# Kernel optimization log

Hardware: AMD Instinct MI355X
Metric: run time of the kernel (lower is better)

Reference implementation:

```python
import jax, jax.numpy as jnp
import numpy as np

S, M, E, K, D = 16384, 512, 16, 2, 256
H1, H2, H3 = 500, 500, 1000


def setup_inputs() -> dict:
    key = jax.random.key(0)
    ks = jax.random.split(key, 8)
    p = lambda k, sh: jax.random.normal(k, sh, dtype=jnp.float32) * 0.02
    return {
        "x": jax.random.normal(ks[0], (S, M), dtype=jnp.float32),
        "noise": jax.random.uniform(ks[1], (S, E), dtype=jnp.float32),  # Router's torch.rand noise
        "Wr": p(ks[2], (E, M)),                       # router weight (Linear, no bias)
        "W1": p(ks[3], (E, M, H1)), "b1": jnp.zeros((E, H1), jnp.float32),
        "W2": p(ks[4], (E, H1, H2)), "b2": jnp.zeros((E, H2), jnp.float32),
        "W3": p(ks[5], (E, H2, H3)), "b3": jnp.zeros((E, H3), jnp.float32),
        "W4": p(ks[6], (E, H3, D)), "b4": jnp.zeros((E, D), jnp.float32),
    }


def reference(x, noise, Wr, W1, b1, W2, b2, W3, b3, W4, b4):
    # Router: zero-init linear + uniform noise
    logits = x @ Wr.T + noise                      # [S,E]
    select = jax.nn.softmax(logits, axis=1)        # [S,E]
    gate, index = jax.lax.top_k(select, K)         # [S,K]
    gate = gate / gate.sum(axis=1, keepdims=True)
    mask = jax.nn.one_hot(index, E, dtype=jnp.float32)  # [S,K,E]

    # load-balance loss
    density = mask.sum(axis=1).mean(axis=0)        # [E]
    density_proxy = select.mean(axis=0)            # [E]
    balance_loss = (density_proxy * density).mean() * float(E ** 2)

    # combine tensor: mask_flat is all-ones, so combine = sum_k gate_k * one_hot_k
    final_weight = (gate[:, :, None] * mask).sum(axis=1)     # [S,E]
    dispatch = (final_weight > 0).astype(x.dtype)            # bool->float, [S,E]
    select0 = dispatch

    # dense one-hot dispatch: expert_inputs[e,s,:] = x[s,:] * dispatch[s,e]
    expert_inputs = jnp.einsum('sm,se->esm', x, dispatch)    # [E,S,M]

    # per-expert Encoder MLP, vectorized over experts
    h = jax.nn.relu(jnp.einsum('esm,emh->esh', expert_inputs, W1) + b1[:, None, :])
    h = jax.nn.relu(jnp.einsum('esh,ehg->esg', h, W2) + b2[:, None, :])
    h = jax.nn.relu(jnp.einsum('esg,egf->esf', h, W3) + b3[:, None, :])
    expert_out = jnp.einsum('esf,efd->esd', h, W4) + b4[:, None, :]  # [E,S,D]

    final_output = jnp.einsum('se,esd->sd', final_weight, expert_out)  # [S,D]
    dist_loss = jnp.float32(0.0)  # t=False path
    return final_output, select0, balance_loss, dist_loss
```

## Files before the change

### kernel.cpp

```cpp
#include <hip/hip_runtime.h>
#include <stdint.h>

#define S_TOK 16384
#define M_DIM 512
#define E_EXP 16
#define D_OUT 256
#define H1D 500
#define H2D 500
#define H3D 1000

typedef float f32x4 __attribute__((ext_vector_type(4)));
typedef long lx2 __attribute__((ext_vector_type(2)));
typedef int i32x2 __attribute__((ext_vector_type(2)));

template <bool HI>
__device__ __forceinline__ int pk8(float a, float b, int old) {
  return __builtin_amdgcn_cvt_pk_fp8_f32(a, b, old, HI);
}
__device__ __forceinline__ unsigned char f2fp8(float f) {
  return (unsigned char)(__builtin_amdgcn_cvt_pk_fp8_f32(f, 0.f, 0, false) & 0xff);
}

__device__ __forceinline__ void ld_lds16(const unsigned char* g, unsigned char* l) {
  __builtin_amdgcn_global_load_lds(
      (const __attribute__((address_space(1))) unsigned int*)(const void*)g,
      (__attribute__((address_space(3))) unsigned int*)(void*)l, 16, 0, 0);
}

struct TokenRec { int i1, i2; float g1, g2; };

__global__ __launch_bounds__(256) void k_router(const float* __restrict__ x,
                                                const float* __restrict__ noise,
                                                const float* __restrict__ Wr,
                                                float* __restrict__ sel_out,
                                                float* __restrict__ sel_buf,
                                                TokenRec* __restrict__ te) {
  __shared__ float wr[E_EXP * 516];
  int t = threadIdx.x;
  for (int i = t; i < E_EXP * M_DIM; i += 256) {
    int e = i >> 9, m = i & 511;
    wr[e * 516 + m] = Wr[i];
  }
  __syncthreads();

  int wv = t >> 6, l = t & 63;
  int e = l & 15, tg = l >> 4;
  int s = blockIdx.x * 16 + wv * 4 + tg;

  const float* xr = x + (size_t)s * M_DIM;
  const float* wre = &wr[e * 516];
  double a0 = 0.0, a1 = 0.0, a2 = 0.0, a3 = 0.0;
#pragma unroll 4
  for (int m = 0; m < M_DIM; m += 4) {
    f32x4 xv = *(const f32x4*)(xr + m);
    f32x4 wv4 = *(const f32x4*)(wre + m);
    a0 += (double)xv.x * (double)wv4.x;
    a1 += (double)xv.y * (double)wv4.y;
    a2 += (double)xv.z * (double)wv4.z;
    a3 += (double)xv.w * (double)wv4.w;
  }
  double a = (a0 + a1) + (a2 + a3);
  a += (double)noise[(size_t)s * E_EXP + e];

  double mx = a;
#pragma unroll
  for (int off = 8; off >= 1; off >>= 1) { double o = __shfl_xor(mx, off, 64); mx = (o > mx) ? o : mx; }
  double p = exp(a - mx);
  double sum = p;
#pragma unroll
  for (int off = 8; off >= 1; off >>= 1) sum += __shfl_xor(sum, off, 64);
  sel_buf[(size_t)s * E_EXP + e] = (float)(p / sum);

  unsigned long long pb = __double_as_longlong(p);
  unsigned long long key = (pb & ~0xFFull) | (unsigned long long)(255 - e);
  unsigned long long k1 = key;
#pragma unroll
  for (int off = 8; off >= 1; off >>= 1) { unsigned long long o = __shfl_xor(k1, off, 64); k1 = (o > k1) ? o : k1; }
  int i1 = 255 - (int)(k1 & 0xFFull);
  unsigned long long key2 = (e == i1) ? 0ull : key;
  unsigned long long k2 = key2;
#pragma unroll
  for (int off = 8; off >= 1; off >>= 1) { unsigned long long o = __shfl_xor(k2, off, 64); k2 = (o > k2) ? o : k2; }
  int i2 = 255 - (int)(k2 & 0xFFull);

  double p1 = __shfl(p, tg * 16 + i1, 64);
  double p2 = __shfl(p, tg * 16 + i2, 64);

  sel_out[(size_t)s * E_EXP + e] = (e == i1 || e == i2) ? 1.f : 0.f;
  if (e == 0) {
    double inv = 1.0 / (p1 + p2);
    TokenRec r; r.i1 = i1; r.i2 = i2; r.g1 = (float)(p1 * inv); r.g2 = (float)(p2 * inv);
    te[s] = r;
  }
}

__global__ __launch_bounds__(256) void k_stats(const float* __restrict__ sel_buf,
                                               const TokenRec* __restrict__ te,
                                               float* __restrict__ partials) {
  __shared__ float psum[256];
  __shared__ unsigned int hist[E_EXP];
  int t = threadIdx.x, b = blockIdx.x;
  if (t < E_EXP) hist[t] = 0u;
  __syncthreads();
  int e = t & 15, rg = t >> 4;
  int base = b * 1024;
  float acc = 0.f;
#pragma unroll 4
  for (int i = 0; i < 64; i++)
    acc += sel_buf[(size_t)(base + i * 16 + rg) * E_EXP + e];
  for (int i = t; i < 1024; i += 256) {
    TokenRec r = te[base + i];
    atomicAdd(&hist[r.i1], 1u);
    atomicAdd(&hist[r.i2], 1u);
  }
  psum[t] = acc;
  __syncthreads();
  if (t < E_EXP) {
    float v = 0.f;
#pragma unroll
    for (int rg2 = 0; rg2 < 16; rg2++) v += psum[rg2 * 16 + t];
    partials[b * 32 + t] = v;
    partials[b * 32 + 16 + t] = (float)hist[t];
  }
}

__global__ void k_prefix_loss(const float* __restrict__ partials,
                              unsigned int* __restrict__ counts,
                              unsigned int* __restrict__ offsets,
                              unsigned int* __restrict__ cursor,
                              float* __restrict__ out_loss) {
  __shared__ float pr[E_EXP];
  __shared__ unsigned int cn[E_EXP];
  int t = threadIdx.x;
  if (t < E_EXP) {
    float p = 0.f, c = 0.f;
    for (int b = 0; b < 16; b++) { p += partials[b * 32 + t]; c += partials[b * 32 + 16 + t]; }
    pr[t] = p; cn[t] = (unsigned int)(c + 0.5f);
    cursor[t] = 0u;
  }
  __syncthreads();
  if (t == 0) {
    unsigned int acc = 0; float ls = 0.f;
    for (int e = 0; e < E_EXP; e++) {
      counts[e] = cn[e];
      offsets[e] = acc;
      acc += cn[e];
      ls += pr[e] * (float)cn[e];
    }
    out_loss[0] = ls * ((float)E_EXP / ((float)S_TOK * (float)S_TOK));
    out_loss[1] = 0.f;
  }
}

__global__ __launch_bounds__(256) void k_listbuild(const TokenRec* __restrict__ te,
                                                   const unsigned int* __restrict__ offsets,
                                                   unsigned int* __restrict__ cursor,
                                                   int* __restrict__ slot_token,
                                                   float* __restrict__ slot_gate,
                                                   int* __restrict__ tok_slot) {
  __shared__ unsigned int lhist[E_EXP];
  __shared__ unsigned int lbase[E_EXP];
  __shared__ unsigned int lcur[E_EXP];
  int t = threadIdx.x, b = blockIdx.x;
  int base = b * 1024;
  if (t < E_EXP) lhist[t] = 0u;
  __syncthreads();
  for (int i = t; i < 1024; i += 256) {
    TokenRec r = te[base + i];
    atomicAdd(&lhist[r.i1], 1u);
    atomicAdd(&lhist[r.i2], 1u);
  }
  __syncthreads();
  if (t < E_EXP) {
    lbase[t] = offsets[t] + atomicAdd(&cursor[t], lhist[t]);
    lcur[t] = 0u;
  }
  __syncthreads();
  for (int i = t; i < 1024; i += 256) {
    int s = base + i;
    TokenRec r = te[s];
    unsigned int p1 = atomicAdd(&lcur[r.i1], 1u);
    int sl1 = (int)(lbase[r.i1] + p1);
    slot_token[sl1] = s; slot_gate[sl1] = r.g1;
    unsigned int p2 = atomicAdd(&lcur[r.i2], 1u);
    int sl2 = (int)(lbase[r.i2] + p2);
    slot_token[sl2] = s; slot_gate[sl2] = r.g2;
    tok_slot[2 * s] = sl1;
    tok_slot[2 * s + 1] = sl2;
  }
}

__global__ __launch_bounds__(256) void k_gather(const float* __restrict__ x,
                                                const int* __restrict__ slot_token,
                                                unsigned char* __restrict__ xg) {
  int idx = blockIdx.x * 256 + threadIdx.x;
  int row = idx >> 6, t6 = idx & 63;
  int blk = t6 >> 3, q = (t6 >> 1) & 3, h = t6 & 1;
  int tkn = slot_token[row];
  const float* xp = x + (size_t)tkn * M_DIM + blk * 64 + h * 32 + q * 8;
  f32x4 v0 = *(const f32x4*)xp;
  f32x4 v1 = *(const f32x4*)(xp + 4);
  int b0 = pk8<false>(v0.x, v0.y, 0); b0 = pk8<true>(v0.z, v0.w, b0);
  int b1 = pk8<false>(v1.x, v1.y, 0); b1 = pk8<true>(v1.z, v1.w, b1);
  i32x2 o; o.x = b0; o.y = b1;
  *(i32x2*)&xg[(size_t)row * 512 + blk * 64 + q * 16 + h * 8] = o;
}

__global__ __launch_bounds__(256) void k_convw_all(const float* __restrict__ W1,
                                                   const float* __restrict__ W2,
                                                   const float* __restrict__ W3,
                                                   const float* __restrict__ W4,
                                                   unsigned char* __restrict__ D1,
                                                   unsigned char* __restrict__ D2,
                                                   unsigned char* __restrict__ D3,
                                                   unsigned char* __restrict__ D4) {
  __shared__ float tile[64][65];
  int tb = blockIdx.x, e = blockIdx.y;
  const float* src; unsigned char* dst;
  int Kr, Nr, Kp, Np, kx, ny;
  if (tb < 64)        { src = W1; dst = D1; Kr = 512;  Nr = H1D; Kp = 512;  Np = 512;  kx = tb >> 3;  ny = tb & 7; }
  else if (tb < 128)  { tb -= 64;  src = W2; dst = D2; Kr = H1D; Nr = H2D; Kp = 512;  Np = 512;  kx = tb >> 3;  ny = tb & 7; }
  else if (tb < 256)  { tb -= 128; src = W3; dst = D3; Kr = H2D; Nr = H3D; Kp = 512;  Np = 1024; kx = tb >> 4;  ny = tb & 15; }
  else                { tb -= 256; src = W4; dst = D4; Kr = H3D; Nr = 256; Kp = 1024; Np = 256;  kx = tb >> 2;  ny = tb & 3; }
  int k0 = kx * 64, n0 = ny * 64;
  int t = threadIdx.x;
  int cx = t & 63, ry = t >> 6;
  const float* sp = src + (size_t)e * Kr * Nr;
#pragma unroll
  for (int i = 0; i < 16; i++) {
    int k = k0 + ry + i * 4, n = n0 + cx;
    float v = (k < Kr && n < Nr) ? sp[(size_t)k * Nr + n] : 0.f;
    tile[ry + i * 4][cx] = v;
  }
  __syncthreads();
  int nl = t >> 2, q = t & 3;
  int b0 = pk8<false>(tile[q * 8 + 0][nl], tile[q * 8 + 1][nl], 0);
  b0 = pk8<true>(tile[q * 8 + 2][nl], tile[q * 8 + 3][nl], b0);
  int b1 = pk8<false>(tile[q * 8 + 4][nl], tile[q * 8 + 5][nl], 0);
  b1 = pk8<true>(tile[q * 8 + 6][nl], tile[q * 8 + 7][nl], b1);
  int c0 = pk8<false>(tile[32 + q * 8 + 0][nl], tile[32 + q * 8 + 1][nl], 0);
  c0 = pk8<true>(tile[32 + q * 8 + 2][nl], tile[32 + q * 8 + 3][nl], c0);
  int c1 = pk8<false>(tile[32 + q * 8 + 4][nl], tile[32 + q * 8 + 5][nl], 0);
  c1 = pk8<true>(tile[32 + q * 8 + 6][nl], tile[32 + q * 8 + 7][nl], c1);
  uint4 pk; pk.x = (unsigned)b0; pk.y = (unsigned)b1; pk.z = (unsigned)c0; pk.w = (unsigned)c1;
  *(uint4*)&dst[(size_t)e * Np * Kp + (size_t)(n0 + nl) * Kp + k0 + q * 16] = pk;
}

__global__ __launch_bounds__(256, 4) void k_gemm_mid(const unsigned char* __restrict__ in,
                                                  const unsigned char* __restrict__ wt,
                                                  const float* __restrict__ bias,
                                                  unsigned char* __restrict__ out,
                                                  const unsigned int* __restrict__ offsets,
                                                  const unsigned int* __restrict__ counts,
                                                  int KP, int NP, int NREAL) {
  int e = blockIdx.z;
  int n_e = (int)counts[e];
  if (n_e == 0) return;
  int base = (int)offsets[e];
  int bn = blockIdx.y;
  __shared__ __align__(16) unsigned char As[2][128 * 64];
  __shared__ __align__(16) unsigned char Bs[2][64 * 64];
  int t = threadIdx.x;
  int w = t >> 6, l = t & 63;
  int wm = w & 1, wn = w >> 1;
  int lr = l & 15, lq = l >> 4;
  int r_ = l >> 2, s_ = l & 3;
  int s2 = s_ ^ ((r_ >> 1) & 3);
  int rsw = (lq ^ ((lr >> 1) & 3)) * 16;
  int c0 = w * 2, c1 = w * 2 + 1;

  unsigned char* dA0[2] = {&As[0][c0 * 1024], &As[1][c0 * 1024]};
  unsigned char* dA1[2] = {&As[0][c1 * 1024], &As[1][c1 * 1024]};
  unsigned char* dB[2]  = {&Bs[0][w * 1024], &Bs[1][w * 1024]};

  const unsigned char* bW = wt + (size_t)e * NP * KP;
  const unsigned char* bsrc = bW + (size_t)(bn * 64 + w * 16 + r_) * KP + s2 * 16;
  int nk = KP >> 6;

  for (int bm = blockIdx.x; bm * 128 < n_e; bm += gridDim.x) {
    int ra = bm * 128 + c0 * 16 + r_; ra = (ra < n_e) ? ra : (n_e - 1);
    int rb = bm * 128 + c1 * 16 + r_; rb = (rb < n_e) ? rb : (n_e - 1);
    const unsigned char* a0 = in + (size_t)(base + ra) * KP + s2 * 16;
    const unsigned char* a1 = in + (size_t)(base + rb) * KP + s2 * 16;
    const unsigned char* bq = bsrc;
    f32x4 acc[4][2];
#pragma unroll
    for (int i = 0; i < 4; i++)
#pragma unroll
      for (int j = 0; j < 2; j++) acc[i][j] = (f32x4){0.f, 0.f, 0.f, 0.f};

    ld_lds16(a0, dA0[0]); ld_lds16(a1, dA1[0]); ld_lds16(bq, dB[0]);
    a0 += 64; a1 += 64; bq += 64;

    for (int ks = 0; ks < nk; ks++) {
      int cb = ks & 1, nb = cb ^ 1;
      __syncthreads();
      if (ks + 1 < nk) {
        ld_lds16(a0, dA0[nb]); ld_lds16(a1, dA1[nb]); ld_lds16(bq, dB[nb]);
        a0 += 64; a1 += 64; bq += 64;
      }
      lx2 af[4], bf[2];
#pragma unroll
      for (int mt = 0; mt < 4; mt++) af[mt] = *(const lx2*)&As[cb][(wm * 64 + mt * 16 + lr) * 64 + rsw];
#pragma unroll
      for (int nt = 0; nt < 2; nt++) bf[nt] = *(const lx2*)&Bs[cb][(wn * 32 + nt * 16 + lr) * 64 + rsw];
#pragma unroll
      for (int mt = 0; mt < 4; mt++)
#pragma unroll
        for (int nt = 0; nt < 2; nt++) {
          acc[mt][nt] = __builtin_amdgcn_mfma_f32_16x16x32_fp8_fp8(af[mt].x, bf[nt].x, acc[mt][nt], 0, 0, 0);
          acc[mt][nt] = __builtin_amdgcn_mfma_f32_16x16x32_fp8_fp8(af[mt].y, bf[nt].y, acc[mt][nt], 0, 0, 0);
        }
    }

#pragma unroll
    for (int nt = 0; nt < 2; nt++) {
      int col = bn * 64 + wn * 32 + nt * 16 + lr;
      bool cok = col < NREAL;
      float bv = cok ? bias[(size_t)e * NREAL + col] : 0.f;
      int kl = col & 63;
      int pb = ((kl >> 3) & 3) * 16 + ((kl >> 5) & 1) * 8 + (kl & 7);
#pragma unroll
      for (int mt = 0; mt < 4; mt++)
#pragma unroll
        for (int reg = 0; reg < 4; reg++) {
          int r = bm * 128 + wm * 64 + mt * 16 + lq * 4 + reg;
          if (r < n_e) {
            float v = cok ? fmaxf(acc[mt][nt][reg] + bv, 0.f) : 0.f;
            out[(size_t)(base + r) * NP + bn * 64 + pb] = f2fp8(v);
          }
        }
    }
  }
}

__global__ __launch_bounds__(256, 4) void k_gemm_fin(const unsigned char* __restrict__ in,
                                                  const unsigned char* __restrict__ wt,
                                                  const float* __restrict__ bias,
                                                  float* __restrict__ eo,
                                                  const unsigned int* __restrict__ offsets,
                                                  const unsigned int* __restrict__ counts,
                                                  const float* __restrict__ slot_gate) {
  const int KP = 1024, NP = 256;
  int e = blockIdx.z;
  int n_e = (int)counts[e];
  if (n_e == 0) return;
  int base = (int)offsets[e];
  int bn = blockIdx.y;
  __shared__ __align__(16) unsigned char As[2][64 * 64];
  __shared__ __align__(16) unsigned char Bs[2][64 * 64];
  int t = threadIdx.x;
  int w = t >> 6, l = t & 63;
  int wm = w & 1, wn = w >> 1;
  int lr = l & 15, lq = l >> 4;
  int r_ = l >> 2, s_ = l & 3;
  int s2 = s_ ^ ((r_ >> 1) & 3);
  int rsw = (lq ^ ((lr >> 1) & 3)) * 16;

  unsigned char* dA[2] = {&As[0][w * 1024], &As[1][w * 1024]};
  unsigned char* dB[2] = {&Bs[0][w * 1024], &Bs[1][w * 1024]};

  const unsigned char* bW = wt + (size_t)e * NP * KP;
  const unsigned char* bsrc = bW + (size_t)(bn * 64 + w * 16 + r_) * KP + s2 * 16;
  int nk = KP >> 6;

  for (int bm = blockIdx.x; bm * 64 < n_e; bm += gridDim.x) {
    int ra = bm * 64 + w * 16 + r_; ra = (ra < n_e) ? ra : (n_e - 1);
    const unsigned char* a0 = in + (size_t)(base + ra) * KP + s2 * 16;
    const unsigned char* bq = bsrc;
    f32x4 acc[2][2];
#pragma unroll
    for (int i = 0; i < 2; i++)
#pragma unroll
      for (int j = 0; j < 2; j++) acc[i][j] = (f32x4){0.f, 0.f, 0.f, 0.f};

    ld_lds16(a0, dA[0]); ld_lds16(bq, dB[0]);
    a0 += 64; bq += 64;

    for (int ks = 0; ks < nk; ks++) {
      int cb = ks & 1, nb = cb ^ 1;
      __syncthreads();
      if (ks + 1 < nk) {
        ld_lds16(a0, dA[nb]); ld_lds16(bq, dB[nb]);
        a0 += 64; bq += 64;
      }
      lx2 af[2], bf[2];
#pragma unroll
      for (int mt = 0; mt < 2; mt++) af[mt] = *(const lx2*)&As[cb][(wm * 32 + mt * 16 + lr) * 64 + rsw];
#pragma unroll
      for (int nt = 0; nt < 2; nt++) bf[nt] = *(const lx2*)&Bs[cb][(wn * 32 + nt * 16 + lr) * 64 + rsw];
#pragma unroll
      for (int mt = 0; mt < 2; mt++)
#pragma unroll
        for (int nt = 0; nt < 2; nt++) {
          acc[mt][nt] = __builtin_amdgcn_mfma_f32_16x16x32_fp8_fp8(af[mt].x, bf[nt].x, acc[mt][nt], 0, 0, 0);
          acc[mt][nt] = __builtin_amdgcn_mfma_f32_16x16x32_fp8_fp8(af[mt].y, bf[nt].y, acc[mt][nt], 0, 0, 0);
        }
    }

#pragma unroll
    for (int mt = 0; mt < 2; mt++)
#pragma unroll
      for (int reg = 0; reg < 4; reg++) {
        int r = bm * 64 + wm * 32 + mt * 16 + lq * 4 + reg;
        if (r < n_e) {
          int gr = base + r;
          float g = slot_gate[gr];
#pragma unroll
          for (int nt = 0; nt < 2; nt++) {
            int col = bn * 64 + wn * 32 + nt * 16 + lr;
            eo[(size_t)gr * NP + col] = g * (acc[mt][nt][reg] + bias[(size_t)e * 256 + col]);
          }
        }
      }
  }
}

__global__ __launch_bounds__(256) void k_combine(const float* __restrict__ eo,
                                                 const int* __restrict__ tok_slot,
                                                 float* __restrict__ out) {
  int idx = blockIdx.x * 256 + threadIdx.x;
  int s = idx >> 6, q = idx & 63;
  int sl1 = tok_slot[2 * s], sl2 = tok_slot[2 * s + 1];
  f32x4 v1 = *(const f32x4*)&eo[(size_t)sl1 * D_OUT + q * 4];
  f32x4 v2 = *(const f32x4*)&eo[(size_t)sl2 * D_OUT + q * 4];
  *(f32x4*)&out[(size_t)s * D_OUT + q * 4] = v1 + v2;
}

extern "C" void kernel_launch(void* const* d_in, const int* in_sizes, int n_in,
                              void* d_out, int out_size, void* d_ws, size_t ws_size,
                              hipStream_t stream) {
  const float* x    = (const float*)d_in[0];
  const float* nois = (const float*)d_in[1];
  const float* Wr   = (const float*)d_in[2];
  const float* W1   = (const float*)d_in[3];
  const float* b1   = (const float*)d_in[4];
  const float* W2   = (const float*)d_in[5];
  const float* b2   = (const float*)d_in[6];
  const float* W3   = (const float*)d_in[7];
  const float* b3   = (const float*)d_in[8];
  const float* W4   = (const float*)d_in[9];
  const float* b4   = (const float*)d_in[10];
  float* out = (float*)d_out;

  char* w = (char*)d_ws;
  unsigned char* actA = (unsigned char*)(w + 0);
  unsigned char* actB = (unsigned char*)(w + 33554432);
  unsigned char* Wt1  = (unsigned char*)(w + 50331648);
  unsigned char* Wt2  = (unsigned char*)(w + 54525952);
  unsigned char* Wt3  = (unsigned char*)(w + 58720256);
  unsigned char* Wt4  = (unsigned char*)(w + 67108864);
  float*         eo   = (float*)(w + 71303168);
  int*           slot_token = (int*)(w + 104857600);
  float*         slot_gate  = (float*)(w + 104988672);
  TokenRec*      te         = (TokenRec*)(w + 105119744);
  unsigned int*  counts  = (unsigned int*)(w + 105381888);
  unsigned int*  cursor  = (unsigned int*)(w + 105381952);
  unsigned int*  offsets = (unsigned int*)(w + 105382016);
  int*           tok_slot = (int*)(w + 105382080);
  float*         sel_buf  = (float*)(w + 0);
  float*         partials = (float*)(w + 1048576);

  float* sel_out  = out + (size_t)S_TOK * D_OUT;
  float* loss_out = out + (size_t)S_TOK * D_OUT + (size_t)S_TOK * E_EXP;

  k_convw_all<<<dim3(320, E_EXP), dim3(256), 0, stream>>>(W1, W2, W3, W4, Wt1, Wt2, Wt3, Wt4);

  k_router<<<dim3(S_TOK / 16), dim3(256), 0, stream>>>(x, nois, Wr, sel_out, sel_buf, te);
  k_stats<<<dim3(16), dim3(256), 0, stream>>>(sel_buf, te, partials);
  k_prefix_loss<<<dim3(1), dim3(64), 0, stream>>>(partials, counts, offsets, cursor, loss_out);
  k_listbuild<<<dim3(16), dim3(256), 0, stream>>>(te, offsets, cursor, slot_token, slot_gate, tok_slot);
  k_gather<<<dim3((2 * S_TOK * 64) / 256), dim3(256), 0, stream>>>(x, slot_token, actB);

  k_gemm_mid<<<dim3(24, 8, E_EXP), dim3(256), 0, stream>>>(actB, Wt1, b1, actA, offsets, counts, 512, 512, H1D);
  k_gemm_mid<<<dim3(24, 8, E_EXP), dim3(256), 0, stream>>>(actA, Wt2, b2, actB, offsets, counts, 512, 512, H2D);
  k_gemm_mid<<<dim3(24, 16, E_EXP), dim3(256), 0, stream>>>(actB, Wt3, b3, actA, offsets, counts, 512, 1024, H3D);
  k_gemm_fin<<<dim3(32, 4, E_EXP), dim3(256), 0, stream>>>(actA, Wt4, b4, eo, offsets, counts, slot_gate);
  k_combine<<<dim3(S_TOK * 64 / 256), dim3(256), 0, stream>>>(eo, tok_slot, out);

  (void)in_sizes; (void)n_in; (void)out_size; (void)ws_size;
}
```

Measured before the change: 382.3 us.

## Enlarge expert GEMM tiles to 128x128 and swap MFMA operands for packed epilogue stores

The middle expert GEMMs now use 128x128 output tiles, where each wave computes a 64x64 sub-tile, and the final GEMM uses 128x64 tiles instead of 64x64. The MFMA operand order is swapped so each lane holds four consecutive output columns. That lets the epilogue write packed 4-byte fp8 words and float4 outputs with vectorised bias loads, replacing scattered single-byte and single-float stores. The goal is more data reuse per LDS load and fewer store instructions. The cost is more accumulator registers, lower occupancy (launch bounds drop to 3) and fewer blocks in the grids.

```diff
diff --git a/kernel.cpp b/kernel.cpp
--- a/kernel.cpp
+++ b/kernel.cpp
@@ -246,13 +246,112 @@
   *(uint4*)&dst[(size_t)e * Np * Kp + (size_t)(n0 + nl) * Kp + k0 + q * 16] = pk;
 }
 
-__global__ __launch_bounds__(256, 4) void k_gemm_mid(const unsigned char* __restrict__ in,
+__global__ __launch_bounds__(256, 3) void k_gemm_mid(const unsigned char* __restrict__ in,
                                                   const unsigned char* __restrict__ wt,
                                                   const float* __restrict__ bias,
                                                   unsigned char* __restrict__ out,
                                                   const unsigned int* __restrict__ offsets,
                                                   const unsigned int* __restrict__ counts,
                                                   int KP, int NP, int NREAL) {
+  int e = blockIdx.z;
+  int n_e = (int)counts[e];
+  if (n_e == 0) return;
+  int base = (int)offsets[e];
+  int bn = blockIdx.y;
+  __shared__ __align__(16) unsigned char As[2][128 * 64];
+  __shared__ __align__(16) unsigned char Bs[2][128 * 64];
+  int t = threadIdx.x;
+  int w = t >> 6, l = t & 63;
+  int wm = w & 1, wn = w >> 1;
+  int lr = l & 15, lq = l >> 4;
+  int r_ = l >> 2, s_ = l & 3;
+  int s2 = s_ ^ ((r_ >> 1) & 3);
+  int rsw = (lq ^ ((lr >> 1) & 3)) * 16;
+  int c0 = 2 * w, c1 = 2 * w + 1;
+
+  unsigned char* dA0[2] = {&As[0][c0 * 1024], &As[1][c0 * 1024]};
+  unsigned char* dA1[2] = {&As[0][c1 * 1024], &As[1][c1 * 1024]};
+  unsigned char* dB0[2] = {&Bs[0][c0 * 1024], &Bs[1][c0 * 1024]};
+  unsigned char* dB1[2] = {&Bs[0][c1 * 1024], &Bs[1][c1 * 1024]};
+
+  const unsigned char* bW = wt + (size_t)e * NP * KP;
+  const unsigned char* bs0 = bW + (size_t)(bn * 128 + c0 * 16 + r_) * KP + s2 * 16;
+  const unsigned char* bs1 = bW + (size_t)(bn * 128 + c1 * 16 + r_) * KP + s2 * 16;
+  int nk = KP >> 6;
+
+  for (int bm = blockIdx.x; bm * 128 < n_e; bm += gridDim.x) {
+    int ra = bm * 128 + c0 * 16 + r_; ra = (ra < n_e) ? ra : (n_e - 1);
+    int rb = bm * 128 + c1 * 16 + r_; rb = (rb < n_e) ? rb : (n_e - 1);
+    const unsigned char* a0 = in + (size_t)(base + ra) * KP + s2 * 16;
+    const unsigned char* a1 = in + (size_t)(base + rb) * KP + s2 * 16;
+    const unsigned char* b0 = bs0;
+    const unsigned char* b1 = bs1;
+    f32x4 acc[4][4];
+#pragma unroll
+    for (int i = 0; i < 4; i++)
+#pragma unroll
+      for (int j = 0; j < 4; j++) acc[i][j] = (f32x4){0.f, 0.f, 0.f, 0.f};
+
+    ld_lds16(a0, dA0[0]); ld_lds16(a1, dA1[0]); ld_lds16(b0, dB0[0]); ld_lds16(b1, dB1[0]);
+    a0 += 64; a1 += 64; b0 += 64; b1 += 64;
+
+    for (int ks = 0; ks < nk; ks++) {
+      int cb = ks & 1, nb = cb ^ 1;
+      __syncthreads();
+      if (ks + 1 < nk) {
+        ld_lds16(a0, dA0[nb]); ld_lds16(a1, dA1[nb]); ld_lds16(b0, dB0[nb]); ld_lds16(b1, dB1[nb]);
+        a0 += 64; a1 += 64; b0 += 64; b1 += 64;
+      }
+      lx2 af[4], wf[4];
+#pragma unroll
+      for (int mi = 0; mi < 4; mi++) af[mi] = *(const lx2*)&As[cb][(wm * 64 + mi * 16 + lr) * 64 + rsw];
+#pragma unroll
+      for (int ni = 0; ni < 4; ni++) wf[ni] = *(const lx2*)&Bs[cb][(wn * 64 + ni * 16 + lr) * 64 + rsw];
+#pragma unroll
+      for (int ni = 0; ni < 4; ni++)
+#pragma unroll
+        for (int mi = 0; mi < 4; mi++) {
+          acc[ni][mi] = __builtin_amdgcn_mfma_f32_16x16x32_fp8_fp8(wf[ni].x, af[mi].x, acc[ni][mi], 0, 0, 0);
+          acc[ni][mi] = __builtin_amdgcn_mfma_f32_16x16x32_fp8_fp8(wf[ni].y, af[mi].y, acc[ni][mi], 0, 0, 0);
+        }
+    }
+
+    int mbase = bm * 128 + wm * 64;
+    int nbase = bn * 128 + wn * 64;
+#pragma unroll
+    for (int ni = 0; ni < 4; ni++) {
+      int n0 = nbase + ni * 16 + lq * 4;
+      bool cok = n0 < NREAL;
+      f32x4 bv = (f32x4){0.f, 0.f, 0.f, 0.f};
+      if (cok) bv = *(const f32x4*)&bias[(size_t)e * NREAL + n0];
+      int k6 = n0 & 63;
+      int off = (n0 >> 6) * 64 + ((k6 >> 3) & 3) * 16 + (k6 >> 5) * 8 + (k6 & 7);
+#pragma unroll
+      for (int mi = 0; mi < 4; mi++) {
+        int m = mbase + mi * 16 + lr;
+        if (m < n_e) {
+          unsigned int pkv = 0u;
+          if (cok) {
+            f32x4 v = acc[ni][mi];
+            int p = pk8<false>(fmaxf(v.x + bv.x, 0.f), fmaxf(v.y + bv.y, 0.f), 0);
+            p = pk8<true>(fmaxf(v.z + bv.z, 0.f), fmaxf(v.w + bv.w, 0.f), p);
+            pkv = (unsigned int)p;
+          }
+          *(unsigned int*)&out[(size_t)(base + m) * NP + off] = pkv;
+        }
+      }
+    }
+  }
+}
+
+__global__ __launch_bounds__(256, 4) void k_gemm_fin(const unsigned char* __restrict__ in,
+                                                  const unsigned char* __restrict__ wt,
+                                                  const float* __restrict__ bias,
+                                                  float* __restrict__ eo,
+                                                  const unsigned int* __restrict__ offsets,
+                                                  const unsigned int* __restrict__ counts,
+                                                  const float* __restrict__ slot_gate) {
+  const int KP = 1024, NP = 256;
   int e = blockIdx.z;
   int n_e = (int)counts[e];
   if (n_e == 0) return;
@@ -267,7 +366,7 @@
   int r_ = l >> 2, s_ = l & 3;
   int s2 = s_ ^ ((r_ >> 1) & 3);
   int rsw = (lq ^ ((lr >> 1) & 3)) * 16;
-  int c0 = w * 2, c1 = w * 2 + 1;
+  int c0 = 2 * w, c1 = 2 * w + 1;
 
   unsigned char* dA0[2] = {&As[0][c0 * 1024], &As[1][c0 * 1024]};
   unsigned char* dA1[2] = {&As[0][c1 * 1024], &As[1][c1 * 1024]};
@@ -283,11 +382,11 @@
     const unsigned char* a0 = in + (size_t)(base + ra) * KP + s2 * 16;
     const unsigned char* a1 = in + (size_t)(base + rb) * KP + s2 * 16;
     const unsigned char* bq = bsrc;
-    f32x4 acc[4][2];
-#pragma unroll
-    for (int i = 0; i < 4; i++)
-#pragma unroll
-      for (int j = 0; j < 2; j++) acc[i][j] = (f32x4){0.f, 0.f, 0.f, 0.f};
+    f32x4 acc[2][4];
+#pragma unroll
+    for (int i = 0; i < 2; i++)
+#pragma unroll
+      for (int j = 0; j < 4; j++) acc[i][j] = (f32x4){0.f, 0.f, 0.f, 0.f};
 
     ld_lds16(a0, dA0[0]); ld_lds16(a1, dA1[0]); ld_lds16(bq, dB[0]);
     a0 += 64; a1 += 64; bq += 64;
@@ -299,120 +398,41 @@
         ld_lds16(a0, dA0[nb]); ld_lds16(a1, dA1[nb]); ld_lds16(bq, dB[nb]);
         a0 += 64; a1 += 64; bq += 64;
       }
-      lx2 af[4], bf[2];
-#pragma unroll
-      for (int mt = 0; mt < 4; mt++) af[mt] = *(const lx2*)&As[cb][(wm * 64 + mt * 16 + lr) * 64 + rsw];
-#pragma unroll
-      for (int nt = 0; nt < 2; nt++) bf[nt] = *(const lx2*)&Bs[cb][(wn * 32 + nt * 16 + lr) * 64 + rsw];
-#pragma unroll
-      for (int mt = 0; mt < 4; mt++)
-#pragma unroll
-        for (int nt = 0; nt < 2; nt++) {
-          acc[mt][nt] = __builtin_amdgcn_mfma_f32_16x16x32_fp8_fp8(af[mt].x, bf[nt].x, acc[mt][nt], 0, 0, 0);
-          acc[mt][nt] = __builtin_amdgcn_mfma_f32_16x16x32_fp8_fp8(af[mt].y, bf[nt].y, acc[mt][nt], 0, 0, 0);
+      lx2 af[4], wf[2];
+#pragma unroll
+      for (int mi = 0; mi < 4; mi++) af[mi] = *(const lx2*)&As[cb][(wm * 64 + mi * 16 + lr) * 64 + rsw];
+#pragma unroll
+      for (int ni = 0; ni < 2; ni++) wf[ni] = *(const lx2*)&Bs[cb][(wn * 32 + ni * 16 + lr) * 64 + rsw];
+#pragma unroll
+      for (int ni = 0; ni < 2; ni++)
+#pragma unroll
+        for (int mi = 0; mi < 4; mi++) {
+          acc[ni][mi] = __builtin_amdgcn_mfma_f32_16x16x32_fp8_fp8(wf[ni].x, af[mi].x, acc[ni][mi], 0, 0, 0);
+          acc[ni][mi] = __builtin_amdgcn_mfma_f32_16x16x32_fp8_fp8(wf[ni].y, af[mi].y, acc[ni][mi], 0, 0, 0);
         }
     }
 
-#pragma unroll
-    for (int nt = 0; nt < 2; nt++) {
-      int col = bn * 64 + wn * 32 + nt * 16 + lr;
-      bool cok = col < NREAL;
-      float bv = cok ? bias[(size_t)e * NREAL + col] : 0.f;
-      int kl = col & 63;
-      int pb = ((kl >> 3) & 3) * 16 + ((kl >> 5) & 1) * 8 + (kl & 7);
-#pragma unroll
-      for (int mt = 0; mt < 4; mt++)
-#pragma unroll
-        for (int reg = 0; reg < 4; reg++) {
-          int r = bm * 128 + wm * 64 + mt * 16 + lq * 4 + reg;
-          if (r < n_e) {
-            float v = cok ? fmaxf(acc[mt][nt][reg] + bv, 0.f) : 0.f;
-            out[(size_t)(base + r) * NP + bn * 64 + pb] = f2fp8(v);
-          }
-        }
-    }
-  }
-}
-
-__global__ __launch_bounds__(256, 4) void k_gemm_fin(const unsigned char* __restrict__ in,
-                                                  const unsigned char* __restrict__ wt,
-                                                  const float* __restrict__ bias,
-                                                  float* __restrict__ eo,
-                                                  const unsigned int* __restrict__ offsets,
-                                                  const unsigned int* __restrict__ counts,
-                                                  const float* __restrict__ slot_gate) {
-  const int KP = 1024, NP = 256;
-  int e = blockIdx.z;
-  int n_e = (int)counts[e];
-  if (n_e == 0) return;
-  int base = (int)offsets[e];
-  int bn = blockIdx.y;
-  __shared__ __align__(16) unsigned char As[2][64 * 64];
-  __shared__ __align__(16) unsigned char Bs[2][64 * 64];
-  int t = threadIdx.x;
-  int w = t >> 6, l = t & 63;
-  int wm = w & 1, wn = w >> 1;
-  int lr = l & 15, lq = l >> 4;
-  int r_ = l >> 2, s_ = l & 3;
-  int s2 = s_ ^ ((r_ >> 1) & 3);
-  int rsw = (lq ^ ((lr >> 1) & 3)) * 16;
-
-  unsigned char* dA[2] = {&As[0][w * 1024], &As[1][w * 1024]};
-  unsigned char* dB[2] = {&Bs[0][w * 1024], &Bs[1][w * 1024]};
-
-  const unsigned char* bW = wt + (size_t)e * NP * KP;
-  const unsigned char* bsrc = bW + (size_t)(bn * 64 + w * 16 + r_) * KP + s2 * 16;
-  int nk = KP >> 6;
-
-  for (int bm = blockIdx.x; bm * 64 < n_e; bm += gridDim.x) {
-    int ra = bm * 64 + w * 16 + r_; ra = (ra < n_e) ? ra : (n_e - 1);
-    const unsigned char* a0 = in + (size_t)(base + ra) * KP + s2 * 16;
-    const unsigned char* bq = bsrc;
-    f32x4 acc[2][2];
-#pragma unroll
-    for (int i = 0; i < 2; i++)
-#pragma unroll
-      for (int j = 0; j < 2; j++) acc[i][j] = (f32x4){0.f, 0.f, 0.f, 0.f};
-
-    ld_lds16(a0, dA[0]); ld_lds16(bq, dB[0]);
-    a0 += 64; bq += 64;
-
-    for (int ks = 0; ks < nk; ks++) {
-      int cb = ks & 1, nb = cb ^ 1;
-      __syncthreads();
-      if (ks + 1 < nk) {
-        ld_lds16(a0, dA[nb]); ld_lds16(bq, dB[nb]);
-        a0 += 64; bq += 64;
-      }
-      lx2 af[2], bf[2];
-#pragma unroll
-      for (int mt = 0; mt < 2; mt++) af[mt] = *(const lx2*)&As[cb][(wm * 32 + mt * 16 + lr) * 64 + rsw];
-#pragma unroll
-      for (int nt = 0; nt < 2; nt++) bf[nt] = *(const lx2*)&Bs[cb][(wn * 32 + nt * 16 + lr) * 64 + rsw];
-#pragma unroll
-      for (int mt = 0; mt < 2; mt++)
-#pragma unroll
-        for (int nt = 0; nt < 2; nt++) {
-          acc[mt][nt] = __builtin_amdgcn_mfma_f32_16x16x32_fp8_fp8(af[mt].x, bf[nt].x, acc[mt][nt], 0, 0, 0);
-          acc[mt][nt] = __builtin_amdgcn_mfma_f32_16x16x32_fp8_fp8(af[mt].y, bf[nt].y, acc[mt][nt], 0, 0, 0);
-        }
-    }
-
-#pragma unroll
-    for (int mt = 0; mt < 2; mt++)
-#pragma unroll
-      for (int reg = 0; reg < 4; reg++) {
-        int r = bm * 64 + wm * 32 + mt * 16 + lq * 4 + reg;
-        if (r < n_e) {
-          int gr = base + r;
+    int mbase = bm * 128 + wm * 64;
+    int nbase = bn * 64 + wn * 32;
+#pragma unroll
+    for (int ni = 0; ni < 2; ni++) {
+      int n0 = nbase + ni * 16 + lq * 4;
+      f32x4 bv = *(const f32x4*)&bias[(size_t)e * 256 + n0];
+#pragma unroll
+      for (int mi = 0; mi < 4; mi++) {
+        int m = mbase + mi * 16 + lr;
+        if (m < n_e) {
+          int gr = base + m;
           float g = slot_gate[gr];
-#pragma unroll
-          for (int nt = 0; nt < 2; nt++) {
-            int col = bn * 64 + wn * 32 + nt * 16 + lr;
-            eo[(size_t)gr * NP + col] = g * (acc[mt][nt][reg] + bias[(size_t)e * 256 + col]);
-          }
+          f32x4 v;
+          v.x = g * (acc[ni][mi].x + bv.x);
+          v.y = g * (acc[ni][mi].y + bv.y);
+          v.z = g * (acc[ni][mi].z + bv.z);
+          v.w = g * (acc[ni][mi].w + bv.w);
+          *(f32x4*)&eo[(size_t)gr * NP + n0] = v;
         }
       }
+    }
   }
 }
 
@@ -472,10 +492,10 @@
   k_listbuild<<<dim3(16), dim3(256), 0, stream>>>(te, offsets, cursor, slot_token, slot_gate, tok_slot);
   k_gather<<<dim3((2 * S_TOK * 64) / 256), dim3(256), 0, stream>>>(x, slot_token, actB);
 
-  k_gemm_mid<<<dim3(24, 8, E_EXP), dim3(256), 0, stream>>>(actB, Wt1, b1, actA, offsets, counts, 512, 512, H1D);
-  k_gemm_mid<<<dim3(24, 8, E_EXP), dim3(256), 0, stream>>>(actA, Wt2, b2, actB, offsets, counts, 512, 512, H2D);
-  k_gemm_mid<<<dim3(24, 16, E_EXP), dim3(256), 0, stream>>>(actB, Wt3, b3, actA, offsets, counts, 512, 1024, H3D);
-  k_gemm_fin<<<dim3(32, 4, E_EXP), dim3(256), 0, stream>>>(actA, Wt4, b4, eo, offsets, counts, slot_gate);
+  k_gemm_mid<<<dim3(16, 4, E_EXP), dim3(256), 0, stream>>>(actB, Wt1, b1, actA, offsets, counts, 512, 512, H1D);
+  k_gemm_mid<<<dim3(16, 4, E_EXP), dim3(256), 0, stream>>>(actA, Wt2, b2, actB, offsets, counts, 512, 512, H2D);
+  k_gemm_mid<<<dim3(16, 8, E_EXP), dim3(256), 0, stream>>>(actB, Wt3, b3, actA, offsets, counts, 512, 1024, H3D);
+  k_gemm_fin<<<dim3(16, 4, E_EXP), dim3(256), 0, stream>>>(actA, Wt4, b4, eo, offsets, counts, slot_gate);
   k_combine<<<dim3(S_TOK * 64 / 256), dim3(256), 0, stream>>>(eo, tok_slot, out);
 
   (void)in_sizes; (void)n_in; (void)out_size; (void)ws_size;
```

Measured after the change: 382.1 us. Within noise of the previous version (-0.1%).
